# Kernel optimization log

Measured on AMD Instinct MI355X. Metric: run time of the kernel, lower is better.

The kernel has to match this reference:

```python
import jax, jax.numpy as jnp
import numpy as np

N, E = 50000, 800000
D, H = 256, 256
OA, OS, OE = 21, 2, 5


def _sage(x, src, dst, wl, bl, wr):
    # PyG SAGEConv: out = lin_l(mean_{j in N(i)} x_j) + lin_r(x_i); bias lives in lin_l
    n = x.shape[0]
    msg = x[src]                                            # [E, d] gather
    agg = jax.ops.segment_sum(msg, dst, num_segments=n)     # [N, d]
    cnt = jax.ops.segment_sum(jnp.ones((src.shape[0],), x.dtype), dst, num_segments=n)
    mean = agg / jnp.maximum(cnt, 1.0)[:, None]
    return mean @ wl.T + bl + x @ wr.T


def _bn(x, g, b, eps=1e-5):
    mu = x.mean(axis=0)
    var = x.var(axis=0)
    return (x - mu) * jax.lax.rsqrt(var + eps) * g + b


def setup_inputs() -> dict:
    key = jax.random.key(0)
    ks = jax.random.split(key, 32)

    def lin(k, o, i):
        s = 1.0 / np.sqrt(i)
        k1, k2 = jax.random.split(k)
        return (jax.random.uniform(k1, (o, i), jnp.float32, -s, s),
                jax.random.uniform(k2, (o,), jnp.float32, -s, s))

    w1l, b1 = lin(ks[3], H, D); w1r, _ = lin(ks[4], H, D)
    w2l, b2 = lin(ks[5], H, H); w2r, _ = lin(ks[6], H, H)
    w3l, b3 = lin(ks[7], H, H); w3r, _ = lin(ks[8], H, H)
    wal, ba = lin(ks[9], OA, H); war, _ = lin(ks[10], OA, H)
    wsl, bs = lin(ks[11], OS, H); wsr, _ = lin(ks[12], OS, H)
    wel, be = lin(ks[13], OE, H); wer, _ = lin(ks[14], OE, H)

    return {
        'x': jax.random.normal(ks[0], (N, D), jnp.float32),
        'edge_src': jax.random.randint(ks[1], (E,), 0, N),
        'edge_dst': jax.random.randint(ks[2], (E,), 0, N),
        'w1l': w1l, 'b1': b1, 'w1r': w1r, 'g1': jnp.ones((H,), jnp.float32), 'bt1': jnp.zeros((H,), jnp.float32),
        'w2l': w2l, 'b2': b2, 'w2r': w2r, 'g2': jnp.ones((H,), jnp.float32), 'bt2': jnp.zeros((H,), jnp.float32),
        'w3l': w3l, 'b3': b3, 'w3r': w3r, 'g3': jnp.ones((H,), jnp.float32), 'bt3': jnp.zeros((H,), jnp.float32),
        'wal': wal, 'ba': ba, 'war': war,
        'wsl': wsl, 'bs': bs, 'wsr': wsr,
        'wel': wel, 'be': be, 'wer': wer,
    }


def reference(x, edge_src, edge_dst,
              w1l, b1, w1r, g1, bt1,
              w2l, b2, w2r, g2, bt2,
              w3l, b3, w3r, g3, bt3,
              wal, ba, war, wsl, bs, wsr, wel, be, wer):
    h = jax.nn.relu(_bn(_sage(x, edge_src, edge_dst, w1l, b1, w1r), g1, bt1))
    h = jax.nn.relu(_bn(_sage(h, edge_src, edge_dst, w2l, b2, w2r), g2, bt2))
    h = jax.nn.relu(_bn(_sage(h, edge_src, edge_dst, w3l, b3, w3r), g3, bt3))
    # dropout is identity in eval mode
    age = _sage(h, edge_src, edge_dst, wal, ba, war)
    sex = _sage(h, edge_src, edge_dst, wsl, bs, wsr)
    eth = _sage(h, edge_src, edge_dst, wel, be, wer)
    return age, sex, eth
```

## Files before the change

### kernel.cpp

```cpp
#include <hip/hip_runtime.h>
#include <hip/hip_bf16.h>
#include <cstddef>

#define HD 256
#define KD 512
#define NH 28

typedef __attribute__((ext_vector_type(8))) short bf16x8;
typedef __attribute__((ext_vector_type(4))) float f32x4;

__device__ inline float bf2f(unsigned short u) { return __uint_as_float(((unsigned)u) << 16); }
__device__ inline unsigned short f2bf(float f) {
    __hip_bfloat16 h = __float2bfloat16(f);
    return *(unsigned short*)&h;
}

__global__ void hist_kernel(const int* __restrict__ dst, int* __restrict__ cnt, int E) {
    int e = blockIdx.x * blockDim.x + threadIdx.x;
    if (e < E) atomicAdd(&cnt[dst[e]], 1);
}

__global__ void chunk_reduce_kernel(const int* __restrict__ cnt, int* __restrict__ bsum, int n) {
    __shared__ int sdata[4];
    int idx = blockIdx.x * 256 + threadIdx.x;
    int v = (idx < n) ? cnt[idx] : 0;
    for (int off = 32; off > 0; off >>= 1) v += __shfl_down(v, off, 64);
    int lane = threadIdx.x & 63, wv = threadIdx.x >> 6;
    if (lane == 0) sdata[wv] = v;
    __syncthreads();
    if (threadIdx.x == 0) bsum[blockIdx.x] = sdata[0] + sdata[1] + sdata[2] + sdata[3];
}

__global__ void scan_chunks_kernel(const int* __restrict__ bsum, int* __restrict__ boff,
                                   int nchunks, int* __restrict__ row_ptr_end, int E) {
    int t = threadIdx.x;
    int v = (t < nchunks) ? bsum[t] : 0;
    int lane = t & 63, wv = t >> 6;
    int incl = v;
    for (int off = 1; off < 64; off <<= 1) { int u = __shfl_up(incl, off, 64); if (lane >= off) incl += u; }
    __shared__ int wsum[4];
    if (lane == 63) wsum[wv] = incl;
    __syncthreads();
    int base = 0;
    for (int w2 = 0; w2 < 4; ++w2) if (w2 < wv) base += wsum[w2];
    if (t < nchunks) boff[t] = base + incl - v;
    if (t == 0) *row_ptr_end = E;
}

__global__ void scan_final_kernel(const int* __restrict__ cnt, const int* __restrict__ boff,
                                  int* __restrict__ row_ptr, float* __restrict__ invdeg, int n) {
    int idx = blockIdx.x * 256 + threadIdx.x;
    int v = (idx < n) ? cnt[idx] : 0;
    int lane = threadIdx.x & 63, wv = threadIdx.x >> 6;
    int incl = v;
    for (int off = 1; off < 64; off <<= 1) { int u = __shfl_up(incl, off, 64); if (lane >= off) incl += u; }
    __shared__ int wsum[4];
    if (lane == 63) wsum[wv] = incl;
    __syncthreads();
    int base = 0;
    for (int w2 = 0; w2 < 4; ++w2) if (w2 < wv) base += wsum[w2];
    if (idx < n) {
        row_ptr[idx] = boff[blockIdx.x] + base + incl - v;
        invdeg[idx] = 1.0f / fmaxf((float)v, 1.0f);
    }
}

__global__ void scatter_kernel(const int* __restrict__ src, const int* __restrict__ dst,
                               const int* __restrict__ row_ptr, int* __restrict__ cursor,
                               int* __restrict__ col_idx, int E) {
    int e = blockIdx.x * blockDim.x + threadIdx.x;
    if (e < E) {
        int d = dst[e];
        int pos = atomicAdd(&cursor[d], 1);
        col_idx[row_ptr[d] + pos] = src[e];
    }
}

__global__ void pack_layer_w(const float* __restrict__ wl, const float* __restrict__ wr,
                             unsigned short* __restrict__ dst) {
    int idx = blockIdx.x * 256 + threadIdx.x;
    if (idx >= HD * KD) return;
    int nn = idx >> 9, k = idx & 511;
    float v = (k < HD) ? wl[nn * HD + k] : wr[nn * HD + (k - HD)];
    dst[idx] = f2bf(v);
}

__global__ void pack_heads2(const float* __restrict__ wal, const float* __restrict__ war,
                            const float* __restrict__ wsl, const float* __restrict__ wsr,
                            const float* __restrict__ wel, const float* __restrict__ wer,
                            const float* __restrict__ ba, const float* __restrict__ bs,
                            const float* __restrict__ be,
                            unsigned short* __restrict__ W2, float* __restrict__ bcat) {
    int idx = blockIdx.x * 256 + threadIdx.x;
    if (idx >= 64 * HD) return;
    int o = idx >> 8, k = idx & 255;
    float v = 0.f;
    if (o < 21)                    v = wal[o * HD + k];
    else if (o < 23)               v = wsl[(o - 21) * HD + k];
    else if (o < 28)               v = wel[(o - 23) * HD + k];
    else if (o >= 32 && o < 53)    v = war[(o - 32) * HD + k];
    else if (o >= 53 && o < 55)    v = wsr[(o - 53) * HD + k];
    else if (o >= 55 && o < 60)    v = wer[(o - 55) * HD + k];
    W2[idx] = f2bf(v);
    if (k == 0 && o < 32) {
        float b = 0.f;
        if (o < 21) b = ba[o]; else if (o < 23) b = bs[o - 21]; else if (o < 28) b = be[o - 23];
        bcat[o] = b;
    }
}

__global__ void convert_x_kernel(const float* __restrict__ x, unsigned short* __restrict__ buf, int n) {
    int idx = blockIdx.x * 256 + threadIdx.x;
    if (idx >= n * 64) return;
    int r = idx >> 6, c4 = (idx & 63) * 4;
    float4 v = ((const float4*)x)[idx];
    ushort4 o;
    o.x = f2bf(v.x); o.y = f2bf(v.y); o.z = f2bf(v.z); o.w = f2bf(v.w);
    *(ushort4*)&buf[(size_t)r * KD + HD + c4] = o;
}

__global__ void agg_mean_bf16(unsigned short* __restrict__ buf,
                              const int* __restrict__ row_ptr, const int* __restrict__ col_idx,
                              const float* __restrict__ invdeg, int n) {
    int half = threadIdx.x >> 5;
    int l32 = threadIdx.x & 31;
    int node = blockIdx.x * 8 + half;
    if (node >= n) return;
    int s = row_ptr[node], e = row_ptr[node + 1];
    int coff = HD + l32 * 8;
    float a[8];
#pragma unroll
    for (int k = 0; k < 8; ++k) a[k] = 0.f;
    int i = s;
    for (; i + 4 <= e; i += 4) {
        int s0 = col_idx[i], s1 = col_idx[i + 1], s2 = col_idx[i + 2], s3 = col_idx[i + 3];
        float4 v0 = *(const float4*)&buf[(size_t)s0 * KD + coff];
        float4 v1 = *(const float4*)&buf[(size_t)s1 * KD + coff];
        float4 v2 = *(const float4*)&buf[(size_t)s2 * KD + coff];
        float4 v3 = *(const float4*)&buf[(size_t)s3 * KD + coff];
        const unsigned short* u0 = (const unsigned short*)&v0;
        const unsigned short* u1 = (const unsigned short*)&v1;
        const unsigned short* u2 = (const unsigned short*)&v2;
        const unsigned short* u3 = (const unsigned short*)&v3;
#pragma unroll
        for (int k = 0; k < 8; ++k) a[k] += bf2f(u0[k]) + bf2f(u1[k]) + bf2f(u2[k]) + bf2f(u3[k]);
    }
    for (; i < e; ++i) {
        int s0 = col_idx[i];
        float4 v = *(const float4*)&buf[(size_t)s0 * KD + coff];
        const unsigned short* u = (const unsigned short*)&v;
#pragma unroll
        for (int k = 0; k < 8; ++k) a[k] += bf2f(u[k]);
    }
    float inv = invdeg[node];
    ushort4 o0, o1;
    o0.x = f2bf(a[0] * inv); o0.y = f2bf(a[1] * inv); o0.z = f2bf(a[2] * inv); o0.w = f2bf(a[3] * inv);
    o1.x = f2bf(a[4] * inv); o1.y = f2bf(a[5] * inv); o1.z = f2bf(a[6] * inv); o1.w = f2bf(a[7] * inv);
    *(ushort4*)&buf[(size_t)node * KD + l32 * 8] = o0;
    *(ushort4*)&buf[(size_t)node * KD + l32 * 8 + 4] = o1;
}

#define SWIZ(row, kc) (((row) << 6) + ((((kc) ^ ((row) & 7))) << 3))

__global__ __launch_bounds__(512) void gemm_mfma_stats(
        const unsigned short* __restrict__ A, const unsigned short* __restrict__ W,
        unsigned short* __restrict__ Zb,
        float* __restrict__ colsum, float* __restrict__ colsumsq, int n) {
    __shared__ __align__(16) short As[128 * 64];
    __shared__ __align__(16) short Bs[256 * 64];
    int t = threadIdx.x;
    int wave = t >> 6, lane = t & 63;
    int wm = wave & 1, wn = wave >> 1;
    int lm = lane & 15, q = lane >> 4;
    int r0 = blockIdx.x * 128;

    f32x4 acc[4][4];
#pragma unroll
    for (int i = 0; i < 4; ++i)
#pragma unroll
        for (int j = 0; j < 4; ++j) acc[i][j] = (f32x4){0.f, 0.f, 0.f, 0.f};

    int srow = t >> 3;
    int skc = t & 7;

    for (int kt = 0; kt < 8; ++kt) {
        int kc = kt * 64;
#pragma unroll
        for (int u = 0; u < 2; ++u) {
            int row = srow + u * 64;
            int ga = r0 + row; if (ga >= n) ga = n - 1;
            *(float4*)&As[SWIZ(row, skc)] = *(const float4*)&A[(size_t)ga * KD + kc + skc * 8];
        }
#pragma unroll
        for (int u = 0; u < 4; ++u) {
            int row = srow + u * 64;
            *(float4*)&Bs[SWIZ(row, skc)] = *(const float4*)&W[(size_t)row * KD + kc + skc * 8];
        }
        __syncthreads();
#pragma unroll
        for (int kk = 0; kk < 2; ++kk) {
            bf16x8 af[4], bfv[4];
#pragma unroll
            for (int i = 0; i < 4; ++i)
                af[i] = *(bf16x8*)&As[SWIZ(wm * 64 + i * 16 + lm, kk * 4 + q)];
#pragma unroll
            for (int j = 0; j < 4; ++j)
                bfv[j] = *(bf16x8*)&Bs[SWIZ(wn * 64 + j * 16 + lm, kk * 4 + q)];
#pragma unroll
            for (int i = 0; i < 4; ++i)
#pragma unroll
                for (int j = 0; j < 4; ++j)
                    acc[i][j] = __builtin_amdgcn_mfma_f32_16x16x32_bf16(af[i], bfv[j], acc[i][j], 0, 0, 0);
        }
        __syncthreads();
    }

    float s[4], s2[4];
#pragma unroll
    for (int j = 0; j < 4; ++j) { s[j] = 0.f; s2[j] = 0.f; }
#pragma unroll
    for (int i = 0; i < 4; ++i) {
        int rbase = r0 + wm * 64 + i * 16 + q * 4;
#pragma unroll
        for (int reg = 0; reg < 4; ++reg) {
            int r = rbase + reg;
            if (r < n) {
#pragma unroll
                for (int j = 0; j < 4; ++j) {
                    float v = acc[i][j][reg];
                    int c = wn * 64 + j * 16 + lm;
                    Zb[(size_t)r * KD + HD + c] = f2bf(v);
                    s[j] += v; s2[j] += v * v;
                }
            }
        }
    }
#pragma unroll
    for (int j = 0; j < 4; ++j) {
        s[j]  += __shfl_xor(s[j], 16, 64);  s[j]  += __shfl_xor(s[j], 32, 64);
        s2[j] += __shfl_xor(s2[j], 16, 64); s2[j] += __shfl_xor(s2[j], 32, 64);
    }
    if (lane < 16) {
#pragma unroll
        for (int j = 0; j < 4; ++j) {
            int c = wn * 64 + j * 16 + lm;
            atomicAdd(&colsum[c], s[j]);
            atomicAdd(&colsumsq[c], s2[j]);
        }
    }
}

__global__ void bn_finalize_kernel(const float* __restrict__ colsum, const float* __restrict__ colsumsq,
                                   const float* __restrict__ g, const float* __restrict__ bt,
                                   float* __restrict__ scale, float* __restrict__ shift, int n) {
    int c = threadIdx.x;
    float fn = (float)n;
    float mu = colsum[c] / fn;
    float var = colsumsq[c] / fn - mu * mu;
    float sc = g[c] / sqrtf(var + 1e-5f);
    scale[c] = sc;
    shift[c] = bt[c] - mu * sc;
}

__global__ void bn_apply_relu_kernel(unsigned short* __restrict__ buf, const float* __restrict__ scale,
                                     const float* __restrict__ shift, int total4) {
    int idx = blockIdx.x * blockDim.x + threadIdx.x;
    if (idx >= total4) return;
    int r = idx >> 6, c4 = (idx & 63) * 4;
    unsigned short* p = &buf[(size_t)r * KD + HD + c4];
    ushort4 z = *(ushort4*)p;
    float4 sc = *(const float4*)&scale[c4];
    float4 sh = *(const float4*)&shift[c4];
    ushort4 o;
    o.x = f2bf(fmaxf(bf2f(z.x) * sc.x + sh.x, 0.f));
    o.y = f2bf(fmaxf(bf2f(z.y) * sc.y + sh.y, 0.f));
    o.z = f2bf(fmaxf(bf2f(z.z) * sc.z + sh.z, 0.f));
    o.w = f2bf(fmaxf(bf2f(z.w) * sc.w + sh.w, 0.f));
    *(ushort4*)p = o;
}

__global__ __launch_bounds__(256) void heads_pgemm(const unsigned short* __restrict__ A,
                                                   const unsigned short* __restrict__ W2,
                                                   unsigned short* __restrict__ PL,
                                                   unsigned short* __restrict__ PR, int n) {
    __shared__ __align__(16) short As[128 * 64];
    __shared__ __align__(16) short Bs[64 * 64];
    int t = threadIdx.x;
    int wave = t >> 6, lane = t & 63;
    int lm = lane & 15, q = lane >> 4;
    int r0 = blockIdx.x * 128;

    f32x4 acc[2][4];
#pragma unroll
    for (int i = 0; i < 2; ++i)
#pragma unroll
        for (int j = 0; j < 4; ++j) acc[i][j] = (f32x4){0.f, 0.f, 0.f, 0.f};

    int srow = t >> 3;
    int skc = t & 7;

    for (int kt = 0; kt < 4; ++kt) {
        int kc = kt * 64;
#pragma unroll
        for (int u = 0; u < 4; ++u) {
            int row = srow + u * 32;
            int ga = r0 + row; if (ga >= n) ga = n - 1;
            *(float4*)&As[SWIZ(row, skc)] = *(const float4*)&A[(size_t)ga * KD + kc + skc * 8];
        }
#pragma unroll
        for (int u = 0; u < 2; ++u) {
            int c = t + u * 256;
            int row = c >> 3, kcc = c & 7;
            *(float4*)&Bs[SWIZ(row, kcc)] = *(const float4*)&W2[(size_t)row * HD + kc + kcc * 8];
        }
        __syncthreads();
#pragma unroll
        for (int kk = 0; kk < 2; ++kk) {
            bf16x8 af[2], bfv[4];
#pragma unroll
            for (int i = 0; i < 2; ++i)
                af[i] = *(bf16x8*)&As[SWIZ(wave * 32 + i * 16 + lm, kk * 4 + q)];
#pragma unroll
            for (int j = 0; j < 4; ++j)
                bfv[j] = *(bf16x8*)&Bs[SWIZ(j * 16 + lm, kk * 4 + q)];
#pragma unroll
            for (int i = 0; i < 2; ++i)
#pragma unroll
                for (int j = 0; j < 4; ++j)
                    acc[i][j] = __builtin_amdgcn_mfma_f32_16x16x32_bf16(af[i], bfv[j], acc[i][j], 0, 0, 0);
        }
        __syncthreads();
    }
#pragma unroll
    for (int i = 0; i < 2; ++i) {
        int rbase = r0 + wave * 32 + i * 16 + q * 4;
#pragma unroll
        for (int reg = 0; reg < 4; ++reg) {
            int r = rbase + reg;
            if (r >= n) continue;
#pragma unroll
            for (int j = 0; j < 4; ++j) {
                int c = j * 16 + lm;
                unsigned short v = f2bf(acc[i][j][reg]);
                if (c < 32) PL[(size_t)r * 32 + c] = v;
                else        PR[(size_t)r * 32 + (c - 32)] = v;
            }
        }
    }
}

__global__ void head_agg(const unsigned short* __restrict__ PL, const unsigned short* __restrict__ PR,
                         const int* __restrict__ row_ptr, const int* __restrict__ col_idx,
                         const float* __restrict__ invdeg, const float* __restrict__ bcat,
                         float* __restrict__ out, int n) {
    int t = threadIdx.x;
    int sub = t >> 4;
    int l16 = t & 15;
    int node = blockIdx.x * 16 + sub;
    if (node >= n) return;
    int s = row_ptr[node], e = row_ptr[node + 1];
    int off = l16 * 2;
    float a0 = 0.f, a1 = 0.f;
    int i = s;
    for (; i + 4 <= e; i += 4) {
        int s0 = col_idx[i], s1 = col_idx[i + 1], s2 = col_idx[i + 2], s3 = col_idx[i + 3];
        unsigned v0 = *(const unsigned*)&PL[(size_t)s0 * 32 + off];
        unsigned v1 = *(const unsigned*)&PL[(size_t)s1 * 32 + off];
        unsigned v2 = *(const unsigned*)&PL[(size_t)s2 * 32 + off];
        unsigned v3 = *(const unsigned*)&PL[(size_t)s3 * 32 + off];
        a0 += bf2f((unsigned short)v0) + bf2f((unsigned short)v1) + bf2f((unsigned short)v2) + bf2f((unsigned short)v3);
        a1 += bf2f((unsigned short)(v0 >> 16)) + bf2f((unsigned short)(v1 >> 16))
            + bf2f((unsigned short)(v2 >> 16)) + bf2f((unsigned short)(v3 >> 16));
    }
    for (; i < e; ++i) {
        unsigned v = *(const unsigned*)&PL[(size_t)col_idx[i] * 32 + off];
        a0 += bf2f((unsigned short)v);
        a1 += bf2f((unsigned short)(v >> 16));
    }
    float inv = invdeg[node];
    unsigned vr = *(const unsigned*)&PR[(size_t)node * 32 + off];
    float o0 = a0 * inv + bf2f((unsigned short)vr) + bcat[off];
    float o1 = a1 * inv + bf2f((unsigned short)(vr >> 16)) + bcat[off + 1];
    int c0 = off, c1 = off + 1;
    if (c0 < 21)      out[(size_t)node * 21 + c0] = o0;
    else if (c0 < 23) out[(size_t)n * 21 + (size_t)node * 2 + (c0 - 21)] = o0;
    else if (c0 < 28) out[(size_t)n * 23 + (size_t)node * 5 + (c0 - 23)] = o0;
    if (c1 < 21)      out[(size_t)node * 21 + c1] = o1;
    else if (c1 < 23) out[(size_t)n * 21 + (size_t)node * 2 + (c1 - 21)] = o1;
    else if (c1 < 28) out[(size_t)n * 23 + (size_t)node * 5 + (c1 - 23)] = o1;
}

static inline char* align256(char* p) {
    return (char*)(((uintptr_t)p + 255) & ~(uintptr_t)255);
}

extern "C" void kernel_launch(void* const* d_in, const int* in_sizes, int n_in,
                              void* d_out, int out_size, void* d_ws, size_t ws_size,
                              hipStream_t stream) {
    const float* x    = (const float*)d_in[0];
    const int*   esrc = (const int*)d_in[1];
    const int*   edst = (const int*)d_in[2];
    const float* w1l = (const float*)d_in[3];  const float* w1r = (const float*)d_in[5];
    const float* g1  = (const float*)d_in[6];  const float* bt1 = (const float*)d_in[7];
    const float* w2l = (const float*)d_in[8];  const float* w2r = (const float*)d_in[10];
    const float* g2  = (const float*)d_in[11]; const float* bt2 = (const float*)d_in[12];
    const float* w3l = (const float*)d_in[13]; const float* w3r = (const float*)d_in[15];
    const float* g3  = (const float*)d_in[16]; const float* bt3 = (const float*)d_in[17];
    const float* wal = (const float*)d_in[18]; const float* ba = (const float*)d_in[19];
    const float* war = (const float*)d_in[20];
    const float* wsl = (const float*)d_in[21]; const float* bs = (const float*)d_in[22];
    const float* wsr = (const float*)d_in[23];
    const float* wel = (const float*)d_in[24]; const float* be = (const float*)d_in[25];
    const float* wer = (const float*)d_in[26];
    float* out = (float*)d_out;

    int N = in_sizes[0] / HD;
    int E = in_sizes[1];

    char* p = (char*)d_ws;
    size_t HB = (size_t)N * KD * sizeof(unsigned short);
    unsigned short* buf0 = (unsigned short*)p; p += HB;
    unsigned short* buf1 = (unsigned short*)p; p += HB;
    p = align256(p);
    unsigned short* PLb = (unsigned short*)p; p += (size_t)N * 32 * sizeof(unsigned short);
    unsigned short* PRb = (unsigned short*)p; p += (size_t)N * 32 * sizeof(unsigned short);
    p = align256(p);
    int* col_idx = (int*)p; p += sizeof(int) * (size_t)E;       p = align256(p);
    int* row_ptr = (int*)p; p += sizeof(int) * (size_t)(N + 1); p = align256(p);
    int* cnt     = (int*)p; p += sizeof(int) * (size_t)N;
    int* cursor  = (int*)p; p += sizeof(int) * (size_t)N;       p = align256(p);
    int* bsum    = (int*)p; p += sizeof(int) * 256;
    int* boff    = (int*)p; p += sizeof(int) * 256;             p = align256(p);
    float* invdeg   = (float*)p; p += sizeof(float) * (size_t)N; p = align256(p);
    float* colsum   = (float*)p; p += sizeof(float) * 256;
    float* colsumsq = (float*)p; p += sizeof(float) * 256;       p = align256(p);
    float* scale    = (float*)p; p += sizeof(float) * 256;
    float* shift    = (float*)p; p += sizeof(float) * 256;       p = align256(p);
    unsigned short* wc1 = (unsigned short*)p; p += sizeof(unsigned short) * HD * KD;
    unsigned short* wc2 = (unsigned short*)p; p += sizeof(unsigned short) * HD * KD;
    unsigned short* wc3 = (unsigned short*)p; p += sizeof(unsigned short) * HD * KD;
    unsigned short* w2h = (unsigned short*)p; p += sizeof(unsigned short) * 64 * HD;
    p = align256(p);
    float* bcat = (float*)p; p += sizeof(float) * 32;
    (void)ws_size; (void)n_in; (void)out_size;

    int nchunks = (N + 255) / 256;

    hipMemsetAsync(cnt, 0, sizeof(int) * 2 * (size_t)N, stream);
    hist_kernel<<<(E + 255) / 256, 256, 0, stream>>>(edst, cnt, E);
    chunk_reduce_kernel<<<nchunks, 256, 0, stream>>>(cnt, bsum, N);
    scan_chunks_kernel<<<1, 256, 0, stream>>>(bsum, boff, nchunks, &row_ptr[N], E);
    scan_final_kernel<<<nchunks, 256, 0, stream>>>(cnt, boff, row_ptr, invdeg, N);
    scatter_kernel<<<(E + 255) / 256, 256, 0, stream>>>(esrc, edst, row_ptr, cursor, col_idx, E);
    pack_layer_w<<<(HD * KD + 255) / 256, 256, 0, stream>>>(w1l, w1r, wc1);
    pack_layer_w<<<(HD * KD + 255) / 256, 256, 0, stream>>>(w2l, w2r, wc2);
    pack_layer_w<<<(HD * KD + 255) / 256, 256, 0, stream>>>(w3l, w3r, wc3);
    pack_heads2<<<(64 * HD + 255) / 256, 256, 0, stream>>>(wal, war, wsl, wsr, wel, wer,
                                                           ba, bs, be, w2h, bcat);
    convert_x_kernel<<<(N * 64 + 255) / 256, 256, 0, stream>>>(x, buf0, N);

    int aggGrid = (N + 7) / 8;
    int gemmGrid = (N + 127) / 128;
    int total4 = N * 64;

    unsigned short* cur = buf0;
    unsigned short* nxt = buf1;
    const unsigned short* wcs[3] = {wc1, wc2, wc3};
    const float* gs[3]  = {g1, g2, g3};
    const float* bts[3] = {bt1, bt2, bt3};

    for (int l = 0; l < 3; ++l) {
        agg_mean_bf16<<<aggGrid, 256, 0, stream>>>(cur, row_ptr, col_idx, invdeg, N);
        hipMemsetAsync(colsum, 0, sizeof(float) * 512, stream);
        gemm_mfma_stats<<<gemmGrid, 512, 0, stream>>>(cur, wcs[l], nxt, colsum, colsumsq, N);
        bn_finalize_kernel<<<1, 256, 0, stream>>>(colsum, colsumsq, gs[l], bts[l], scale, shift, N);
        bn_apply_relu_kernel<<<(total4 + 255) / 256, 256, 0, stream>>>(nxt, scale, shift, total4);
        unsigned short* t2 = cur; cur = nxt; nxt = t2;
    }

    heads_pgemm<<<gemmGrid, 256, 0, stream>>>(cur + HD, w2h, PLb, PRb, N);
    head_agg<<<(N + 15) / 16, 256, 0, stream>>>(PLb, PRb, row_ptr, col_idx, invdeg, bcat, out, N);
}
```

Baseline: 571.4 us.

## Pad CSR rows to multiples of eight, widen aggregation, split GEMM columns

```diff
diff --git a/kernel.cpp b/kernel.cpp
--- a/kernel.cpp
+++ b/kernel.cpp
@@ -23,7 +23,7 @@
 __global__ void chunk_reduce_kernel(const int* __restrict__ cnt, int* __restrict__ bsum, int n) {
     __shared__ int sdata[4];
     int idx = blockIdx.x * 256 + threadIdx.x;
-    int v = (idx < n) ? cnt[idx] : 0;
+    int v = (idx < n) ? ((cnt[idx] + 7) & ~7) : 0;
     for (int off = 32; off > 0; off >>= 1) v += __shfl_down(v, off, 64);
     int lane = threadIdx.x & 63, wv = threadIdx.x >> 6;
     if (lane == 0) sdata[wv] = v;
@@ -32,7 +32,7 @@
 }
 
 __global__ void scan_chunks_kernel(const int* __restrict__ bsum, int* __restrict__ boff,
-                                   int nchunks, int* __restrict__ row_ptr_end, int E) {
+                                   int nchunks, int* __restrict__ row_ptr_end) {
     int t = threadIdx.x;
     int v = (t < nchunks) ? bsum[t] : 0;
     int lane = t & 63, wv = t >> 6;
@@ -44,15 +44,16 @@
     int base = 0;
     for (int w2 = 0; w2 < 4; ++w2) if (w2 < wv) base += wsum[w2];
     if (t < nchunks) boff[t] = base + incl - v;
-    if (t == 0) *row_ptr_end = E;
+    if (t == nchunks - 1) *row_ptr_end = base + incl;
 }
 
 __global__ void scan_final_kernel(const int* __restrict__ cnt, const int* __restrict__ boff,
                                   int* __restrict__ row_ptr, float* __restrict__ invdeg, int n) {
     int idx = blockIdx.x * 256 + threadIdx.x;
     int v = (idx < n) ? cnt[idx] : 0;
+    int pv = (v + 7) & ~7;
     int lane = threadIdx.x & 63, wv = threadIdx.x >> 6;
-    int incl = v;
+    int incl = pv;
     for (int off = 1; off < 64; off <<= 1) { int u = __shfl_up(incl, off, 64); if (lane >= off) incl += u; }
     __shared__ int wsum[4];
     if (lane == 63) wsum[wv] = incl;
@@ -60,7 +61,7 @@
     int base = 0;
     for (int w2 = 0; w2 < 4; ++w2) if (w2 < wv) base += wsum[w2];
     if (idx < n) {
-        row_ptr[idx] = boff[blockIdx.x] + base + incl - v;
+        row_ptr[idx] = boff[blockIdx.x] + base + incl - pv;
         invdeg[idx] = 1.0f / fmaxf((float)v, 1.0f);
     }
 }
@@ -74,6 +75,15 @@
         int pos = atomicAdd(&cursor[d], 1);
         col_idx[row_ptr[d] + pos] = src[e];
     }
+}
+
+__global__ void fill_pad_kernel(const int* __restrict__ cnt, const int* __restrict__ row_ptr,
+                                int* __restrict__ col_idx, int n) {
+    int idx = blockIdx.x * 256 + threadIdx.x;
+    if (idx >= n) return;
+    int s = row_ptr[idx] + cnt[idx];
+    int e = row_ptr[idx + 1];
+    for (; s < e; ++s) col_idx[s] = n;
 }
 
 __global__ void pack_layer_w(const float* __restrict__ wl, const float* __restrict__ wr,
@@ -119,60 +129,63 @@
     *(ushort4*)&buf[(size_t)r * KD + HD + c4] = o;
 }
 
-__global__ void agg_mean_bf16(unsigned short* __restrict__ buf,
-                              const int* __restrict__ row_ptr, const int* __restrict__ col_idx,
-                              const float* __restrict__ invdeg, int n) {
-    int half = threadIdx.x >> 5;
-    int l32 = threadIdx.x & 31;
-    int node = blockIdx.x * 8 + half;
+__global__ __launch_bounds__(256) void agg_mean8(unsigned short* __restrict__ buf,
+                                                 const int* __restrict__ row_ptr,
+                                                 const int* __restrict__ col_idx,
+                                                 const float* __restrict__ invdeg, int n) {
+    int wv = threadIdx.x >> 6, lane = threadIdx.x & 63;
+    int node = blockIdx.x * 4 + wv;
     if (node >= n) return;
     int s = row_ptr[node], e = row_ptr[node + 1];
-    int coff = HD + l32 * 8;
-    float a[8];
-#pragma unroll
-    for (int k = 0; k < 8; ++k) a[k] = 0.f;
-    int i = s;
-    for (; i + 4 <= e; i += 4) {
-        int s0 = col_idx[i], s1 = col_idx[i + 1], s2 = col_idx[i + 2], s3 = col_idx[i + 3];
-        float4 v0 = *(const float4*)&buf[(size_t)s0 * KD + coff];
-        float4 v1 = *(const float4*)&buf[(size_t)s1 * KD + coff];
-        float4 v2 = *(const float4*)&buf[(size_t)s2 * KD + coff];
-        float4 v3 = *(const float4*)&buf[(size_t)s3 * KD + coff];
-        const unsigned short* u0 = (const unsigned short*)&v0;
-        const unsigned short* u1 = (const unsigned short*)&v1;
-        const unsigned short* u2 = (const unsigned short*)&v2;
-        const unsigned short* u3 = (const unsigned short*)&v3;
-#pragma unroll
-        for (int k = 0; k < 8; ++k) a[k] += bf2f(u0[k]) + bf2f(u1[k]) + bf2f(u2[k]) + bf2f(u3[k]);
-    }
-    for (; i < e; ++i) {
-        int s0 = col_idx[i];
-        float4 v = *(const float4*)&buf[(size_t)s0 * KD + coff];
-        const unsigned short* u = (const unsigned short*)&v;
-#pragma unroll
-        for (int k = 0; k < 8; ++k) a[k] += bf2f(u[k]);
+    const unsigned short* src = buf + HD + lane * 4;
+    float a0 = 0.f, a1 = 0.f, a2 = 0.f, a3 = 0.f;
+    for (int i = s; i < e; i += 8) {
+        int4 ja = *(const int4*)&col_idx[i];
+        int4 jb = *(const int4*)&col_idx[i + 4];
+        uint2 r0 = *(const uint2*)(src + (size_t)ja.x * KD);
+        uint2 r1 = *(const uint2*)(src + (size_t)ja.y * KD);
+        uint2 r2 = *(const uint2*)(src + (size_t)ja.z * KD);
+        uint2 r3 = *(const uint2*)(src + (size_t)ja.w * KD);
+        uint2 r4 = *(const uint2*)(src + (size_t)jb.x * KD);
+        uint2 r5 = *(const uint2*)(src + (size_t)jb.y * KD);
+        uint2 r6 = *(const uint2*)(src + (size_t)jb.z * KD);
+        uint2 r7 = *(const uint2*)(src + (size_t)jb.w * KD);
+        a0 += __uint_as_float(r0.x << 16); a1 += __uint_as_float(r0.x & 0xffff0000u);
+        a2 += __uint_as_float(r0.y << 16); a3 += __uint_as_float(r0.y & 0xffff0000u);
+        a0 += __uint_as_float(r1.x << 16); a1 += __uint_as_float(r1.x & 0xffff0000u);
+        a2 += __uint_as_float(r1.y << 16); a3 += __uint_as_float(r1.y & 0xffff0000u);
+        a0 += __uint_as_float(r2.x << 16); a1 += __uint_as_float(r2.x & 0xffff0000u);
+        a2 += __uint_as_float(r2.y << 16); a3 += __uint_as_float(r2.y & 0xffff0000u);
+        a0 += __uint_as_float(r3.x << 16); a1 += __uint_as_float(r3.x & 0xffff0000u);
+        a2 += __uint_as_float(r3.y << 16); a3 += __uint_as_float(r3.y & 0xffff0000u);
+        a0 += __uint_as_float(r4.x << 16); a1 += __uint_as_float(r4.x & 0xffff0000u);
+        a2 += __uint_as_float(r4.y << 16); a3 += __uint_as_float(r4.y & 0xffff0000u);
+        a0 += __uint_as_float(r5.x << 16); a1 += __uint_as_float(r5.x & 0xffff0000u);
+        a2 += __uint_as_float(r5.y << 16); a3 += __uint_as_float(r5.y & 0xffff0000u);
+        a0 += __uint_as_float(r6.x << 16); a1 += __uint_as_float(r6.x & 0xffff0000u);
+        a2 += __uint_as_float(r6.y << 16); a3 += __uint_as_float(r6.y & 0xffff0000u);
+        a0 += __uint_as_float(r7.x << 16); a1 += __uint_as_float(r7.x & 0xffff0000u);
+        a2 += __uint_as_float(r7.y << 16); a3 += __uint_as_float(r7.y & 0xffff0000u);
     }
     float inv = invdeg[node];
-    ushort4 o0, o1;
-    o0.x = f2bf(a[0] * inv); o0.y = f2bf(a[1] * inv); o0.z = f2bf(a[2] * inv); o0.w = f2bf(a[3] * inv);
-    o1.x = f2bf(a[4] * inv); o1.y = f2bf(a[5] * inv); o1.z = f2bf(a[6] * inv); o1.w = f2bf(a[7] * inv);
-    *(ushort4*)&buf[(size_t)node * KD + l32 * 8] = o0;
-    *(ushort4*)&buf[(size_t)node * KD + l32 * 8 + 4] = o1;
+    ushort4 o;
+    o.x = f2bf(a0 * inv); o.y = f2bf(a1 * inv); o.z = f2bf(a2 * inv); o.w = f2bf(a3 * inv);
+    *(ushort4*)&buf[(size_t)node * KD + lane * 4] = o;
 }
 
 #define SWIZ(row, kc) (((row) << 6) + ((((kc) ^ ((row) & 7))) << 3))
 
-__global__ __launch_bounds__(512) void gemm_mfma_stats(
+__global__ __launch_bounds__(256) void gemm_mfma_stats(
         const unsigned short* __restrict__ A, const unsigned short* __restrict__ W,
         unsigned short* __restrict__ Zb,
         float* __restrict__ colsum, float* __restrict__ colsumsq, int n) {
     __shared__ __align__(16) short As[128 * 64];
-    __shared__ __align__(16) short Bs[256 * 64];
+    __shared__ __align__(16) short Bs[128 * 64];
     int t = threadIdx.x;
     int wave = t >> 6, lane = t & 63;
     int wm = wave & 1, wn = wave >> 1;
     int lm = lane & 15, q = lane >> 4;
-    int r0 = blockIdx.x * 128;
+    int r0 = blockIdx.x * 128, c0 = blockIdx.y * 128;
 
     f32x4 acc[4][4];
 #pragma unroll
@@ -186,15 +199,11 @@
     for (int kt = 0; kt < 8; ++kt) {
         int kc = kt * 64;
 #pragma unroll
-        for (int u = 0; u < 2; ++u) {
-            int row = srow + u * 64;
+        for (int u = 0; u < 4; ++u) {
+            int row = srow + u * 32;
             int ga = r0 + row; if (ga >= n) ga = n - 1;
             *(float4*)&As[SWIZ(row, skc)] = *(const float4*)&A[(size_t)ga * KD + kc + skc * 8];
-        }
-#pragma unroll
-        for (int u = 0; u < 4; ++u) {
-            int row = srow + u * 64;
-            *(float4*)&Bs[SWIZ(row, skc)] = *(const float4*)&W[(size_t)row * KD + kc + skc * 8];
+            *(float4*)&Bs[SWIZ(row, skc)] = *(const float4*)&W[(size_t)(c0 + row) * KD + kc + skc * 8];
         }
         __syncthreads();
 #pragma unroll
@@ -228,7 +237,7 @@
 #pragma unroll
                 for (int j = 0; j < 4; ++j) {
                     float v = acc[i][j][reg];
-                    int c = wn * 64 + j * 16 + lm;
+                    int c = c0 + wn * 64 + j * 16 + lm;
                     Zb[(size_t)r * KD + HD + c] = f2bf(v);
                     s[j] += v; s2[j] += v * v;
                 }
@@ -240,13 +249,21 @@
         s[j]  += __shfl_xor(s[j], 16, 64);  s[j]  += __shfl_xor(s[j], 32, 64);
         s2[j] += __shfl_xor(s2[j], 16, 64); s2[j] += __shfl_xor(s2[j], 32, 64);
     }
+    float* red = (float*)As;
+    if (t < 128) { red[t * 2] = 0.f; red[t * 2 + 1] = 0.f; }
+    __syncthreads();
     if (lane < 16) {
 #pragma unroll
         for (int j = 0; j < 4; ++j) {
-            int c = wn * 64 + j * 16 + lm;
-            atomicAdd(&colsum[c], s[j]);
-            atomicAdd(&colsumsq[c], s2[j]);
-        }
+            int cl = wn * 64 + j * 16 + lm;
+            atomicAdd(&red[cl * 2], s[j]);
+            atomicAdd(&red[cl * 2 + 1], s2[j]);
+        }
+    }
+    __syncthreads();
+    if (t < 128) {
+        atomicAdd(&colsum[c0 + t], red[t * 2]);
+        atomicAdd(&colsumsq[c0 + t], red[t * 2 + 1]);
     }
 }
 
@@ -361,8 +378,7 @@
     int s = row_ptr[node], e = row_ptr[node + 1];
     int off = l16 * 2;
     float a0 = 0.f, a1 = 0.f;
-    int i = s;
-    for (; i + 4 <= e; i += 4) {
+    for (int i = s; i < e; i += 4) {
         int s0 = col_idx[i], s1 = col_idx[i + 1], s2 = col_idx[i + 2], s3 = col_idx[i + 3];
         unsigned v0 = *(const unsigned*)&PL[(size_t)s0 * 32 + off];
         unsigned v1 = *(const unsigned*)&PL[(size_t)s1 * 32 + off];
@@ -371,11 +387,6 @@
         a0 += bf2f((unsigned short)v0) + bf2f((unsigned short)v1) + bf2f((unsigned short)v2) + bf2f((unsigned short)v3);
         a1 += bf2f((unsigned short)(v0 >> 16)) + bf2f((unsigned short)(v1 >> 16))
             + bf2f((unsigned short)(v2 >> 16)) + bf2f((unsigned short)(v3 >> 16));
-    }
-    for (; i < e; ++i) {
-        unsigned v = *(const unsigned*)&PL[(size_t)col_idx[i] * 32 + off];
-        a0 += bf2f((unsigned short)v);
-        a1 += bf2f((unsigned short)(v >> 16));
     }
     float inv = invdeg[node];
     unsigned vr = *(const unsigned*)&PR[(size_t)node * 32 + off];
@@ -418,14 +429,14 @@
     int E = in_sizes[1];
 
     char* p = (char*)d_ws;
-    size_t HB = (size_t)N * KD * sizeof(unsigned short);
+    size_t HB = (size_t)(N + 1) * KD * sizeof(unsigned short);
     unsigned short* buf0 = (unsigned short*)p; p += HB;
     unsigned short* buf1 = (unsigned short*)p; p += HB;
     p = align256(p);
-    unsigned short* PLb = (unsigned short*)p; p += (size_t)N * 32 * sizeof(unsigned short);
+    unsigned short* PLb = (unsigned short*)p; p += (size_t)(N + 1) * 32 * sizeof(unsigned short);
     unsigned short* PRb = (unsigned short*)p; p += (size_t)N * 32 * sizeof(unsigned short);
     p = align256(p);
-    int* col_idx = (int*)p; p += sizeof(int) * (size_t)E;       p = align256(p);
+    int* col_idx = (int*)p; p += sizeof(int) * ((size_t)E + 8 * (size_t)N + 64);  p = align256(p);
     int* row_ptr = (int*)p; p += sizeof(int) * (size_t)(N + 1); p = align256(p);
     int* cnt     = (int*)p; p += sizeof(int) * (size_t)N;
     int* cursor  = (int*)p; p += sizeof(int) * (size_t)N;       p = align256(p);
@@ -447,11 +458,15 @@
     int nchunks = (N + 255) / 256;
 
     hipMemsetAsync(cnt, 0, sizeof(int) * 2 * (size_t)N, stream);
+    hipMemsetAsync(buf0 + (size_t)N * KD, 0, KD * sizeof(unsigned short), stream);
+    hipMemsetAsync(buf1 + (size_t)N * KD, 0, KD * sizeof(unsigned short), stream);
+    hipMemsetAsync(PLb + (size_t)N * 32, 0, 32 * sizeof(unsigned short), stream);
     hist_kernel<<<(E + 255) / 256, 256, 0, stream>>>(edst, cnt, E);
     chunk_reduce_kernel<<<nchunks, 256, 0, stream>>>(cnt, bsum, N);
-    scan_chunks_kernel<<<1, 256, 0, stream>>>(bsum, boff, nchunks, &row_ptr[N], E);
+    scan_chunks_kernel<<<1, 256, 0, stream>>>(bsum, boff, nchunks, &row_ptr[N]);
     scan_final_kernel<<<nchunks, 256, 0, stream>>>(cnt, boff, row_ptr, invdeg, N);
     scatter_kernel<<<(E + 255) / 256, 256, 0, stream>>>(esrc, edst, row_ptr, cursor, col_idx, E);
+    fill_pad_kernel<<<nchunks, 256, 0, stream>>>(cnt, row_ptr, col_idx, N);
     pack_layer_w<<<(HD * KD + 255) / 256, 256, 0, stream>>>(w1l, w1r, wc1);
     pack_layer_w<<<(HD * KD + 255) / 256, 256, 0, stream>>>(w2l, w2r, wc2);
     pack_layer_w<<<(HD * KD + 255) / 256, 256, 0, stream>>>(w3l, w3r, wc3);
@@ -459,8 +474,8 @@
                                                            ba, bs, be, w2h, bcat);
     convert_x_kernel<<<(N * 64 + 255) / 256, 256, 0, stream>>>(x, buf0, N);
 
-    int aggGrid = (N + 7) / 8;
-    int gemmGrid = (N + 127) / 128;
+    int aggGrid = (N + 3) / 4;
+    dim3 gemmGrid((N + 127) / 128, 2);
     int total4 = N * 64;
 
     unsigned short* cur = buf0;
@@ -470,14 +485,14 @@
     const float* bts[3] = {bt1, bt2, bt3};
 
     for (int l = 0; l < 3; ++l) {
-        agg_mean_bf16<<<aggGrid, 256, 0, stream>>>(cur, row_ptr, col_idx, invdeg, N);
+        agg_mean8<<<aggGrid, 256, 0, stream>>>(cur, row_ptr, col_idx, invdeg, N);
         hipMemsetAsync(colsum, 0, sizeof(float) * 512, stream);
-        gemm_mfma_stats<<<gemmGrid, 512, 0, stream>>>(cur, wcs[l], nxt, colsum, colsumsq, N);
+        gemm_mfma_stats<<<gemmGrid, 256, 0, stream>>>(cur, wcs[l], nxt, colsum, colsumsq, N);
         bn_finalize_kernel<<<1, 256, 0, stream>>>(colsum, colsumsq, gs[l], bts[l], scale, shift, N);
         bn_apply_relu_kernel<<<(total4 + 255) / 256, 256, 0, stream>>>(nxt, scale, shift, total4);
         unsigned short* t2 = cur; cur = nxt; nxt = t2;
     }
 
-    heads_pgemm<<<gemmGrid, 256, 0, stream>>>(cur + HD, w2h, PLb, PRb, N);
+    heads_pgemm<<<(N + 127) / 128, 256, 0, stream>>>(cur + HD, w2h, PLb, PRb, N);
     head_agg<<<(N + 15) / 16, 256, 0, stream>>>(PLb, PRb, row_ptr, col_idx, invdeg, bcat, out, N);
 }
```

New measurement: 586.4 us. 1.03x slower.
